# Performance work log

Hardware: AMD Instinct MI355X
Metric: run time of the kernel (lower is better)

Reference implementation:

```python
import jax, jax.numpy as jnp
import numpy as np

HIDDEN = 4096
K = 4          # Gibbs sampling steps
LR = 0.01
IMG = (16, 64, 64, 3)  # batch, H, W, C


def setup_inputs() -> dict:
    key = jax.random.key(0)
    k1, k2 = jax.random.split(key)
    inputs = jax.random.uniform(k1, IMG, dtype=jnp.float32)
    flat = IMG[1] * IMG[2] * IMG[3]
    # GlorotNormal init: std = sqrt(2 / (fan_in + fan_out))
    scale = (2.0 / (flat + HIDDEN)) ** 0.5
    W = jax.random.normal(k2, (flat, HIDDEN), dtype=jnp.float32) * scale
    a = jnp.zeros((flat, 1), dtype=jnp.float32)
    b = jnp.zeros((HIDDEN, 1), dtype=jnp.float32)
    return {"inputs": inputs, "W": W, "a": a, "b": b}


def reference(inputs, W, a, b):
    B = inputs.shape[0]
    flat = inputs.shape[1] * inputs.shape[2] * inputs.shape[3]
    vs = inputs.reshape(B, flat, 1)  # each sample is a (flat,1) column vector

    def per_sample(carry, v):
        W, a, b = carry
        v_init = v
        # k Gibbs steps: h = sigma(b + W^T v); v = sigma(a + W h)
        h = None
        for _ in range(K):
            h = jax.nn.sigmoid(b + W.T @ v)
            v = jax.nn.sigmoid(a + W @ h)
        h_init = jax.nn.sigmoid(b + W.T @ v_init)
        # Contrastive divergence with .assign (replace, not accumulate) as in source
        W_new = LR * (v_init @ h_init.T - v @ h.T)
        a_new = LR * (v_init - v)
        b_new = LR * (h_init - h)
        return (W_new, a_new, b_new), v

    _, vs_out = jax.lax.scan(per_sample, (W, a, b), vs)
    # call() returns self.v, i.e. the reconstruction of the LAST batch element
    return vs_out[-1]
```

## Files before the change

kernel.cpp:

```cpp
#include <hip/hip_runtime.h>
#include <math.h>

#define FLAT 12288
#define NH   4096
#define KSTEPS 4
#define LRC 0.01f
#define NSEG 384
#define RPS  32
#define WSCALE 64.0f
#define WINV   0.015625f

typedef float v2f __attribute__((ext_vector_type(2)));

__device__ __forceinline__ float sigm(float x) {
    return __builtin_amdgcn_rcpf(1.0f + __expf(-x));
}

template <int CTRL>
__device__ __forceinline__ float dpp_add(float x) {
    int s = __builtin_amdgcn_update_dpp(0, __float_as_int(x), CTRL, 0xf, 0xf, true);
    return x + __int_as_float(s);
}
__device__ __forceinline__ float wave_sum63(float x) {
    x = dpp_add<0x111>(x);
    x = dpp_add<0x112>(x);
    x = dpp_add<0x114>(x);
    x = dpp_add<0x118>(x);
    x = dpp_add<0x142>(x);
    x = dpp_add<0x143>(x);
    return x;
}


__global__ __launch_bounds__(256) void k_colpart_cvt(const float* __restrict__ W,
                                                     const float* __restrict__ v,
                                                     float* __restrict__ partials,
                                                     unsigned int* __restrict__ W8) {
    const float4* W4 = (const float4*)W;
    int c4 = blockIdx.x * 256 + threadIdx.x;
    int r0 = blockIdx.y * RPS;
    float4 acc = make_float4(0.f, 0.f, 0.f, 0.f);
    for (int r = r0; r < r0 + RPS; ++r) {
        float vr = v[r];
        float4 w = W4[(size_t)r * (NH / 4) + c4];
        acc.x = fmaf(w.x, vr, acc.x);
        acc.y = fmaf(w.y, vr, acc.y);
        acc.z = fmaf(w.z, vr, acc.z);
        acc.w = fmaf(w.w, vr, acc.w);
        unsigned int p = 0;
        p = __builtin_amdgcn_cvt_pk_fp8_f32(w.x * WSCALE, w.y * WSCALE, p, false);
        p = __builtin_amdgcn_cvt_pk_fp8_f32(w.z * WSCALE, w.w * WSCALE, p, true);
        W8[(size_t)r * (NH / 4) + c4] = p;
    }
    ((float4*)partials)[(size_t)blockIdx.y * (NH / 4) + c4] = acc;
}

__global__ __launch_bounds__(256) void k_colpart_fp8(const uint4* __restrict__ W8,
                                                     const float* __restrict__ v,
                                                     float* __restrict__ partials) {
    int c16 = threadIdx.x;
    int r0 = blockIdx.x * RPS;
    float acc[16];
#pragma unroll
    for (int i = 0; i < 16; i++) acc[i] = 0.f;
    for (int r = r0; r < r0 + RPS; ++r) {
        float vr = v[r] * WINV;
        uint4 w = W8[(size_t)r * (NH / 16) + c16];
        v2f f;
        f = __builtin_amdgcn_cvt_pk_f32_fp8(w.x, false); acc[0]  = fmaf(f.x, vr, acc[0]);  acc[1]  = fmaf(f.y, vr, acc[1]);
        f = __builtin_amdgcn_cvt_pk_f32_fp8(w.x, true);  acc[2]  = fmaf(f.x, vr, acc[2]);  acc[3]  = fmaf(f.y, vr, acc[3]);
        f = __builtin_amdgcn_cvt_pk_f32_fp8(w.y, false); acc[4]  = fmaf(f.x, vr, acc[4]);  acc[5]  = fmaf(f.y, vr, acc[5]);
        f = __builtin_amdgcn_cvt_pk_f32_fp8(w.y, true);  acc[6]  = fmaf(f.x, vr, acc[6]);  acc[7]  = fmaf(f.y, vr, acc[7]);
        f = __builtin_amdgcn_cvt_pk_f32_fp8(w.z, false); acc[8]  = fmaf(f.x, vr, acc[8]);  acc[9]  = fmaf(f.y, vr, acc[9]);
        f = __builtin_amdgcn_cvt_pk_f32_fp8(w.z, true);  acc[10] = fmaf(f.x, vr, acc[10]); acc[11] = fmaf(f.y, vr, acc[11]);
        f = __builtin_amdgcn_cvt_pk_f32_fp8(w.w, false); acc[12] = fmaf(f.x, vr, acc[12]); acc[13] = fmaf(f.y, vr, acc[13]);
        f = __builtin_amdgcn_cvt_pk_f32_fp8(w.w, true);  acc[14] = fmaf(f.x, vr, acc[14]); acc[15] = fmaf(f.y, vr, acc[15]);
    }
    float4* P = (float4*)(partials + (size_t)blockIdx.x * NH + (size_t)c16 * 16);
#pragma unroll
    for (int q = 0; q < 4; q++) {
        float4 o; o.x = acc[4*q]; o.y = acc[4*q+1]; o.z = acc[4*q+2]; o.w = acc[4*q+3];
        P[q] = o;
    }
}

__global__ __launch_bounds__(256) void k_hreduce(const float* __restrict__ partials,
                                                 const float* __restrict__ b,
                                                 float* __restrict__ h,
                                                 float* __restrict__ hi,
                                                 int nseg) {
    int c  = threadIdx.x & 31;
    int sg = threadIdx.x >> 5;
    int col = blockIdx.x * 32 + c;
    float s = 0.f;
    for (int g = sg; g < nseg; g += 8) s += partials[(size_t)g * NH + col];
    __shared__ float red[8][33];
    red[sg][c] = s;
    __syncthreads();
    if (threadIdx.x < 32) {
        float t = 0.f;
#pragma unroll
        for (int g2 = 0; g2 < 8; g2++) t += red[g2][threadIdx.x];
        float hh = sigm(t + b[col]);
        h[col] = hh;
        if (hi) hi[col] = hh;
    }
}

__global__ __launch_bounds__(256) void k_vstep_fp8(const unsigned char* __restrict__ W8,
                                                   const float* __restrict__ h,
                                                   const float* __restrict__ a,
                                                   float* __restrict__ v) {
    int wid = threadIdx.x >> 6, lane = threadIdx.x & 63;
    int row = blockIdx.x * 4 + wid;
    const uint4* Wr = (const uint4*)(W8 + (size_t)row * NH);
    const float4* h4 = (const float4*)h;
    float acc = 0.f;
    for (int k = lane; k < NH / 16; k += 64) {
        uint4 w = Wr[k];
        float4 h0 = h4[4*k], h1 = h4[4*k+1], h2 = h4[4*k+2], h3 = h4[4*k+3];
        v2f f;
        f = __builtin_amdgcn_cvt_pk_f32_fp8(w.x, false); acc = fmaf(f.x, h0.x, acc); acc = fmaf(f.y, h0.y, acc);
        f = __builtin_amdgcn_cvt_pk_f32_fp8(w.x, true);  acc = fmaf(f.x, h0.z, acc); acc = fmaf(f.y, h0.w, acc);
        f = __builtin_amdgcn_cvt_pk_f32_fp8(w.y, false); acc = fmaf(f.x, h1.x, acc); acc = fmaf(f.y, h1.y, acc);
        f = __builtin_amdgcn_cvt_pk_f32_fp8(w.y, true);  acc = fmaf(f.x, h1.z, acc); acc = fmaf(f.y, h1.w, acc);
        f = __builtin_amdgcn_cvt_pk_f32_fp8(w.z, false); acc = fmaf(f.x, h2.x, acc); acc = fmaf(f.y, h2.y, acc);
        f = __builtin_amdgcn_cvt_pk_f32_fp8(w.z, true);  acc = fmaf(f.x, h2.z, acc); acc = fmaf(f.y, h2.w, acc);
        f = __builtin_amdgcn_cvt_pk_f32_fp8(w.w, false); acc = fmaf(f.x, h3.x, acc); acc = fmaf(f.y, h3.y, acc);
        f = __builtin_amdgcn_cvt_pk_f32_fp8(w.w, true);  acc = fmaf(f.x, h3.z, acc); acc = fmaf(f.y, h3.w, acc);
    }
    acc = wave_sum63(acc);
    if (lane == 63) v[row] = sigm(a[row] + acc * WINV);
}


#define TB  512
#define RVB (FLAT / TB)
#define RHB (NH / TB)
#define NWAVES (TB / 64)

__global__ __launch_bounds__(512) void k_phaseB(const float* __restrict__ inputs,
                                                const float* __restrict__ hi0,
                                                const float* __restrict__ hk0,
                                                const float* __restrict__ vk0,
                                                float* __restrict__ out) {
    int t = threadIdx.x;
    int lane = t & 63, wid = t >> 6;
    __shared__ float2 red[2][NWAVES];

    float Vi[RVB], Vk[RVB], v[RVB], Vn[RVB];
    float Hi[RHB], Hk[RHB], h[RHB], hini[RHB];

#pragma unroll
    for (int r = 0; r < RVB; r++) { int i = r * TB + t; Vi[r] = inputs[i]; Vk[r] = vk0[i]; }
#pragma unroll
    for (int r = 0; r < RHB; r++) { int j = r * TB + t; Hi[r] = hi0[j]; Hk[r] = hk0[j]; }

    int rc = 0;
    for (int s = 1; s < 16; ++s) {
        const float* vin = inputs + (size_t)s * FLAT;
#pragma unroll
        for (int r = 0; r < RVB; r++) { Vn[r] = vin[r * TB + t]; v[r] = Vn[r]; }

        for (int k = 0; k < KSTEPS; ++k) {
            float px0 = 0.f, px1 = 0.f, px2 = 0.f, px3 = 0.f;
            float py0 = 0.f, py1 = 0.f, py2 = 0.f, py3 = 0.f;
#pragma unroll
            for (int r = 0; r < RVB; r += 4) {
                px0 = fmaf(Vi[r],   v[r],   px0); py0 = fmaf(Vk[r],   v[r],   py0);
                px1 = fmaf(Vi[r+1], v[r+1], px1); py1 = fmaf(Vk[r+1], v[r+1], py1);
                px2 = fmaf(Vi[r+2], v[r+2], px2); py2 = fmaf(Vk[r+2], v[r+2], py2);
                px3 = fmaf(Vi[r+3], v[r+3], px3); py3 = fmaf(Vk[r+3], v[r+3], py3);
            }
            float px = wave_sum63((px0 + px1) + (px2 + px3));
            float py = wave_sum63((py0 + py1) + (py2 + py3));
            if (lane == 63) { float2 w2; w2.x = px; w2.y = py; red[rc & 1][wid] = w2; }
            __syncthreads();
            float al, be;
            {
                const float4* R4 = (const float4*)&red[rc & 1][0];
                float4 r0 = R4[0], r1 = R4[1], r2 = R4[2], r3 = R4[3];
                al = (r0.x + r1.x) + (r2.x + r3.x) + ((r0.z + r1.z) + (r2.z + r3.z));
                be = (r0.y + r1.y) + (r2.y + r3.y) + ((r0.w + r1.w) + (r2.w + r3.w));
            }
            rc++;
            float ca = LRC * (1.f + al), cb = LRC * (1.f + be);

            float qx0 = 0.f, qx1 = 0.f, qy0 = 0.f, qy1 = 0.f;
#pragma unroll
            for (int r = 0; r < RHB; r += 2) {
                float h0 = sigm(ca * Hi[r]   - cb * Hk[r]);
                float h1 = sigm(ca * Hi[r+1] - cb * Hk[r+1]);
                h[r] = h0; h[r+1] = h1;
                if (k == 0) { hini[r] = h0; hini[r+1] = h1; }
                qx0 = fmaf(Hi[r],   h0, qx0); qy0 = fmaf(Hk[r],   h0, qy0);
                qx1 = fmaf(Hi[r+1], h1, qx1); qy1 = fmaf(Hk[r+1], h1, qy1);
            }
            float qx = wave_sum63(qx0 + qx1), qy = wave_sum63(qy0 + qy1);
            if (lane == 63) { float2 w2; w2.x = qx; w2.y = qy; red[rc & 1][wid] = w2; }
            __syncthreads();
            float ga, de;
            {
                const float4* R4 = (const float4*)&red[rc & 1][0];
                float4 r0 = R4[0], r1 = R4[1], r2 = R4[2], r3 = R4[3];
                ga = (r0.x + r1.x) + (r2.x + r3.x) + ((r0.z + r1.z) + (r2.z + r3.z));
                de = (r0.y + r1.y) + (r2.y + r3.y) + ((r0.w + r1.w) + (r2.w + r3.w));
            }
            rc++;
            float cg = LRC * (1.f + ga), cd = LRC * (1.f + de);

#pragma unroll
            for (int r = 0; r < RVB; r++) v[r] = sigm(cg * Vi[r] - cd * Vk[r]);
        }

#pragma unroll
        for (int r = 0; r < RVB; r++) { Vk[r] = v[r]; Vi[r] = Vn[r]; }
#pragma unroll
        for (int r = 0; r < RHB; r++) { Hk[r] = h[r]; Hi[r] = hini[r]; }
    }

#pragma unroll
    for (int r = 0; r < RVB; r++) out[r * TB + t] = Vk[r];
}


extern "C" void kernel_launch(void* const* d_in, const int* in_sizes, int n_in,
                              void* d_out, int out_size, void* d_ws, size_t ws_size,
                              hipStream_t stream) {
    const float* inputs = (const float*)d_in[0];
    const float* W      = (const float*)d_in[1];
    const float* a_in   = (const float*)d_in[2];
    const float* b_in   = (const float*)d_in[3];
    float* out = (float*)d_out;

    unsigned int* W8 = (unsigned int*)d_ws;
    float* partials = (float*)((char*)d_ws + (size_t)FLAT * NH);
    float* h  = partials + (size_t)NSEG * NH;
    float* hi = h + NH;
    float* v  = hi + NH;

    dim3 blk(256);

    k_colpart_cvt<<<dim3(4, NSEG), blk, 0, stream>>>(W, inputs, partials, W8);
    k_hreduce<<<dim3(NH / 32), blk, 0, stream>>>(partials, b_in, h, hi, NSEG);
    k_vstep_fp8<<<dim3(FLAT / 4), blk, 0, stream>>>((const unsigned char*)W8, h, a_in, v);

    for (int k = 1; k < KSTEPS; ++k) {
        k_colpart_fp8<<<dim3(NSEG), blk, 0, stream>>>((const uint4*)W8, v, partials);
        k_hreduce<<<dim3(NH / 32), blk, 0, stream>>>(partials, b_in, h, (float*)nullptr, NSEG);
        k_vstep_fp8<<<dim3(FLAT / 4), blk, 0, stream>>>((const unsigned char*)W8, h, a_in, v);
    }

    k_phaseB<<<1, TB, 0, stream>>>(inputs, hi, h, v, out);
}
```

Before: 536.4 us.

## Fuse v-step and next h-partial pass into one kernel reusing FP8 W rows

Combines the v = sigmoid(a + W h) row pass with the following W^T v column-partial pass. Each wave loads an FP8 row once, computes its v element, and immediately accumulates that row's contribution to the hidden partials. This halves the FP8 weight reads per Gibbs step and removes one launch per step. In exchange it keeps 64 accumulators per thread, which adds register pressure and can lower occupancy, and it doubles the number of partial segments that k_hreduce must sum.

Result: no change. 545.1 us (+1.6%).

```diff
diff --git a/kernel.cpp b/kernel.cpp
--- a/kernel.cpp
+++ b/kernel.cpp
@@ -7,6 +7,7 @@
 #define LRC 0.01f
 #define NSEG 384
 #define RPS  32
+#define NSEGF 768
 #define WSCALE 64.0f
 #define WINV   0.015625f
 
@@ -29,6 +30,32 @@
     x = dpp_add<0x142>(x);
     x = dpp_add<0x143>(x);
     return x;
+}
+
+__device__ __forceinline__ float dot16(uint4 w, const float4* __restrict__ h4, int k) {
+    float4 ha = h4[4*k+0], hb = h4[4*k+1], hc = h4[4*k+2], hd = h4[4*k+3];
+    v2f f; float d = 0.f;
+    f = __builtin_amdgcn_cvt_pk_f32_fp8(w.x, false); d = fmaf(f.x, ha.x, d); d = fmaf(f.y, ha.y, d);
+    f = __builtin_amdgcn_cvt_pk_f32_fp8(w.x, true);  d = fmaf(f.x, ha.z, d); d = fmaf(f.y, ha.w, d);
+    f = __builtin_amdgcn_cvt_pk_f32_fp8(w.y, false); d = fmaf(f.x, hb.x, d); d = fmaf(f.y, hb.y, d);
+    f = __builtin_amdgcn_cvt_pk_f32_fp8(w.y, true);  d = fmaf(f.x, hb.z, d); d = fmaf(f.y, hb.w, d);
+    f = __builtin_amdgcn_cvt_pk_f32_fp8(w.z, false); d = fmaf(f.x, hc.x, d); d = fmaf(f.y, hc.y, d);
+    f = __builtin_amdgcn_cvt_pk_f32_fp8(w.z, true);  d = fmaf(f.x, hc.z, d); d = fmaf(f.y, hc.w, d);
+    f = __builtin_amdgcn_cvt_pk_f32_fp8(w.w, false); d = fmaf(f.x, hd.x, d); d = fmaf(f.y, hd.y, d);
+    f = __builtin_amdgcn_cvt_pk_f32_fp8(w.w, true);  d = fmaf(f.x, hd.z, d); d = fmaf(f.y, hd.w, d);
+    return d;
+}
+
+__device__ __forceinline__ void accum16(uint4 w, float vs, float* acc) {
+    v2f f;
+    f = __builtin_amdgcn_cvt_pk_f32_fp8(w.x, false); acc[0]  = fmaf(f.x, vs, acc[0]);  acc[1]  = fmaf(f.y, vs, acc[1]);
+    f = __builtin_amdgcn_cvt_pk_f32_fp8(w.x, true);  acc[2]  = fmaf(f.x, vs, acc[2]);  acc[3]  = fmaf(f.y, vs, acc[3]);
+    f = __builtin_amdgcn_cvt_pk_f32_fp8(w.y, false); acc[4]  = fmaf(f.x, vs, acc[4]);  acc[5]  = fmaf(f.y, vs, acc[5]);
+    f = __builtin_amdgcn_cvt_pk_f32_fp8(w.y, true);  acc[6]  = fmaf(f.x, vs, acc[6]);  acc[7]  = fmaf(f.y, vs, acc[7]);
+    f = __builtin_amdgcn_cvt_pk_f32_fp8(w.z, false); acc[8]  = fmaf(f.x, vs, acc[8]);  acc[9]  = fmaf(f.y, vs, acc[9]);
+    f = __builtin_amdgcn_cvt_pk_f32_fp8(w.z, true);  acc[10] = fmaf(f.x, vs, acc[10]); acc[11] = fmaf(f.y, vs, acc[11]);
+    f = __builtin_amdgcn_cvt_pk_f32_fp8(w.w, false); acc[12] = fmaf(f.x, vs, acc[12]); acc[13] = fmaf(f.y, vs, acc[13]);
+    f = __builtin_amdgcn_cvt_pk_f32_fp8(w.w, true);  acc[14] = fmaf(f.x, vs, acc[14]); acc[15] = fmaf(f.y, vs, acc[15]);
 }
 
 
@@ -55,35 +82,6 @@
     ((float4*)partials)[(size_t)blockIdx.y * (NH / 4) + c4] = acc;
 }
 
-__global__ __launch_bounds__(256) void k_colpart_fp8(const uint4* __restrict__ W8,
-                                                     const float* __restrict__ v,
-                                                     float* __restrict__ partials) {
-    int c16 = threadIdx.x;
-    int r0 = blockIdx.x * RPS;
-    float acc[16];
-#pragma unroll
-    for (int i = 0; i < 16; i++) acc[i] = 0.f;
-    for (int r = r0; r < r0 + RPS; ++r) {
-        float vr = v[r] * WINV;
-        uint4 w = W8[(size_t)r * (NH / 16) + c16];
-        v2f f;
-        f = __builtin_amdgcn_cvt_pk_f32_fp8(w.x, false); acc[0]  = fmaf(f.x, vr, acc[0]);  acc[1]  = fmaf(f.y, vr, acc[1]);
-        f = __builtin_amdgcn_cvt_pk_f32_fp8(w.x, true);  acc[2]  = fmaf(f.x, vr, acc[2]);  acc[3]  = fmaf(f.y, vr, acc[3]);
-        f = __builtin_amdgcn_cvt_pk_f32_fp8(w.y, false); acc[4]  = fmaf(f.x, vr, acc[4]);  acc[5]  = fmaf(f.y, vr, acc[5]);
-        f = __builtin_amdgcn_cvt_pk_f32_fp8(w.y, true);  acc[6]  = fmaf(f.x, vr, acc[6]);  acc[7]  = fmaf(f.y, vr, acc[7]);
-        f = __builtin_amdgcn_cvt_pk_f32_fp8(w.z, false); acc[8]  = fmaf(f.x, vr, acc[8]);  acc[9]  = fmaf(f.y, vr, acc[9]);
-        f = __builtin_amdgcn_cvt_pk_f32_fp8(w.z, true);  acc[10] = fmaf(f.x, vr, acc[10]); acc[11] = fmaf(f.y, vr, acc[11]);
-        f = __builtin_amdgcn_cvt_pk_f32_fp8(w.w, false); acc[12] = fmaf(f.x, vr, acc[12]); acc[13] = fmaf(f.y, vr, acc[13]);
-        f = __builtin_amdgcn_cvt_pk_f32_fp8(w.w, true);  acc[14] = fmaf(f.x, vr, acc[14]); acc[15] = fmaf(f.y, vr, acc[15]);
-    }
-    float4* P = (float4*)(partials + (size_t)blockIdx.x * NH + (size_t)c16 * 16);
-#pragma unroll
-    for (int q = 0; q < 4; q++) {
-        float4 o; o.x = acc[4*q]; o.y = acc[4*q+1]; o.z = acc[4*q+2]; o.w = acc[4*q+3];
-        P[q] = o;
-    }
-}
-
 __global__ __launch_bounds__(256) void k_hreduce(const float* __restrict__ partials,
                                                  const float* __restrict__ b,
                                                  float* __restrict__ h,
@@ -107,6 +105,78 @@
     }
 }
 
+__global__ __launch_bounds__(256) void k_vh_fused(const unsigned char* __restrict__ W8,
+                                                  const float* __restrict__ h,
+                                                  const float* __restrict__ a,
+                                                  float* __restrict__ partials) {
+    int lane = threadIdx.x & 63, wid = threadIdx.x >> 6;
+    int row0 = blockIdx.x * 16 + wid * 4;
+    const float4* h4 = (const float4*)h;
+    __shared__ float pbuf[2][NH];
+
+    float acc[64];
+#pragma unroll
+    for (int i = 0; i < 64; i++) acc[i] = 0.f;
+
+    for (int rr = 0; rr < 4; ++rr) {
+        int row = row0 + rr;
+        const uint4* Wr = (const uint4*)(W8 + (size_t)row * NH);
+        uint4 w0 = Wr[lane], w1 = Wr[lane + 64], w2 = Wr[lane + 128], w3 = Wr[lane + 192];
+        float d0 = dot16(w0, h4, lane);
+        float d1 = dot16(w1, h4, lane + 64);
+        float d2 = dot16(w2, h4, lane + 128);
+        float d3 = dot16(w3, h4, lane + 192);
+        float s = wave_sum63((d0 + d1) + (d2 + d3));
+        s = __int_as_float(__builtin_amdgcn_readlane(__float_as_int(s), 63));
+        float vr = sigm(a[row] + s * WINV);
+        float vs = vr * WINV;
+        accum16(w0, vs, acc);
+        accum16(w1, vs, acc + 16);
+        accum16(w2, vs, acc + 32);
+        accum16(w3, vs, acc + 48);
+    }
+
+    if (wid < 2) {
+#pragma unroll
+        for (int i = 0; i < 4; i++) {
+            float4* dst = (float4*)&pbuf[wid][16 * (lane + 64 * i)];
+            dst[0] = make_float4(acc[16*i+0],  acc[16*i+1],  acc[16*i+2],  acc[16*i+3]);
+            dst[1] = make_float4(acc[16*i+4],  acc[16*i+5],  acc[16*i+6],  acc[16*i+7]);
+            dst[2] = make_float4(acc[16*i+8],  acc[16*i+9],  acc[16*i+10], acc[16*i+11]);
+            dst[3] = make_float4(acc[16*i+12], acc[16*i+13], acc[16*i+14], acc[16*i+15]);
+        }
+    }
+    __syncthreads();
+    if (wid >= 2) {
+#pragma unroll
+        for (int i = 0; i < 4; i++) {
+            float4* p = (float4*)&pbuf[wid - 2][16 * (lane + 64 * i)];
+#pragma unroll
+            for (int q = 0; q < 4; q++) {
+                float4 t = p[q];
+                t.x += acc[16*i + 4*q + 0];
+                t.y += acc[16*i + 4*q + 1];
+                t.z += acc[16*i + 4*q + 2];
+                t.w += acc[16*i + 4*q + 3];
+                p[q] = t;
+            }
+        }
+    }
+    __syncthreads();
+    {
+        int c0 = threadIdx.x * 16;
+        float4* out4 = (float4*)(partials + (size_t)blockIdx.x * NH + c0);
+        const float4* p0 = (const float4*)&pbuf[0][c0];
+        const float4* p1 = (const float4*)&pbuf[1][c0];
+#pragma unroll
+        for (int q = 0; q < 4; q++) {
+            float4 x = p0[q], y = p1[q];
+            x.x += y.x; x.y += y.y; x.z += y.z; x.w += y.w;
+            out4[q] = x;
+        }
+    }
+}
+
 __global__ __launch_bounds__(256) void k_vstep_fp8(const unsigned char* __restrict__ W8,
                                                    const float* __restrict__ h,
                                                    const float* __restrict__ a,
@@ -117,17 +187,7 @@
     const float4* h4 = (const float4*)h;
     float acc = 0.f;
     for (int k = lane; k < NH / 16; k += 64) {
-        uint4 w = Wr[k];
-        float4 h0 = h4[4*k], h1 = h4[4*k+1], h2 = h4[4*k+2], h3 = h4[4*k+3];
-        v2f f;
-        f = __builtin_amdgcn_cvt_pk_f32_fp8(w.x, false); acc = fmaf(f.x, h0.x, acc); acc = fmaf(f.y, h0.y, acc);
-        f = __builtin_amdgcn_cvt_pk_f32_fp8(w.x, true);  acc = fmaf(f.x, h0.z, acc); acc = fmaf(f.y, h0.w, acc);
-        f = __builtin_amdgcn_cvt_pk_f32_fp8(w.y, false); acc = fmaf(f.x, h1.x, acc); acc = fmaf(f.y, h1.y, acc);
-        f = __builtin_amdgcn_cvt_pk_f32_fp8(w.y, true);  acc = fmaf(f.x, h1.z, acc); acc = fmaf(f.y, h1.w, acc);
-        f = __builtin_amdgcn_cvt_pk_f32_fp8(w.z, false); acc = fmaf(f.x, h2.x, acc); acc = fmaf(f.y, h2.y, acc);
-        f = __builtin_amdgcn_cvt_pk_f32_fp8(w.z, true);  acc = fmaf(f.x, h2.z, acc); acc = fmaf(f.y, h2.w, acc);
-        f = __builtin_amdgcn_cvt_pk_f32_fp8(w.w, false); acc = fmaf(f.x, h3.x, acc); acc = fmaf(f.y, h3.y, acc);
-        f = __builtin_amdgcn_cvt_pk_f32_fp8(w.w, true);  acc = fmaf(f.x, h3.z, acc); acc = fmaf(f.y, h3.w, acc);
+        acc += dot16(Wr[k], h4, k);
     }
     acc = wave_sum63(acc);
     if (lane == 63) v[row] = sigm(a[row] + acc * WINV);
@@ -235,7 +295,7 @@
 
     unsigned int* W8 = (unsigned int*)d_ws;
     float* partials = (float*)((char*)d_ws + (size_t)FLAT * NH);
-    float* h  = partials + (size_t)NSEG * NH;
+    float* h  = partials + (size_t)NSEGF * NH;
     float* hi = h + NH;
     float* v  = hi + NH;
 
@@ -243,13 +303,13 @@
 
     k_colpart_cvt<<<dim3(4, NSEG), blk, 0, stream>>>(W, inputs, partials, W8);
     k_hreduce<<<dim3(NH / 32), blk, 0, stream>>>(partials, b_in, h, hi, NSEG);
+
+    for (int k = 1; k < KSTEPS; ++k) {
+        k_vh_fused<<<dim3(FLAT / 16), blk, 0, stream>>>((const unsigned char*)W8, h, a_in, partials);
+        k_hreduce<<<dim3(NH / 32), blk, 0, stream>>>(partials, b_in, h, (float*)nullptr, NSEGF);
+    }
+
     k_vstep_fp8<<<dim3(FLAT / 4), blk, 0, stream>>>((const unsigned char*)W8, h, a_in, v);
 
-    for (int k = 1; k < KSTEPS; ++k) {
-        k_colpart_fp8<<<dim3(NSEG), blk, 0, stream>>>((const uint4*)W8, v, partials);
-        k_hreduce<<<dim3(NH / 32), blk, 0, stream>>>(partials, b_in, h, (float*)nullptr, NSEG);
-        k_vstep_fp8<<<dim3(FLAT / 4), blk, 0, stream>>>((const unsigned char*)W8, h, a_in, v);
-    }
-
     k_phaseB<<<1, TB, 0, stream>>>(inputs, hi, h, v, out);
 }
```
